# Performance work log

Measured on AMD Instinct MI355X. Metric: run time of the kernel, lower is better.

## Reference

```python
import jax, jax.numpy as jnp
import numpy as np

D, H, F, N, V, B, S, T = 512, 8, 2048, 2, 32000, 2, 1024, 1024


def _pe(seq_len, d):
    pos = np.arange(seq_len)[:, None].astype(np.float32)
    div = np.exp(np.arange(0, d, 2).astype(np.float32) * (-np.log(10000.0) / d))
    pe = np.zeros((seq_len, d), np.float32)
    pe[:, 0::2] = np.sin(pos * div)
    pe[:, 1::2] = np.cos(pos * div)
    return jnp.asarray(pe)


def _ln(x, g, b, eps=1e-6):
    # torch .var() default is unbiased (ddof=1)
    m = x.mean(-1, keepdims=True)
    v = jnp.sum((x - m) ** 2, -1, keepdims=True) / (x.shape[-1] - 1)
    return g * (x - m) / jnp.sqrt(v + eps) + b


def _mha(q, k, v, mask, w, b):
    # w: [4, D, D] (q,k,v,o); b: [4, D]
    Bq, Sq, Dm = q.shape
    Sk = k.shape[1]
    dk = Dm // H
    Q = (q @ w[0] + b[0]).reshape(Bq, Sq, H, dk).transpose(0, 2, 1, 3)
    K = (k @ w[1] + b[1]).reshape(Bq, Sk, H, dk).transpose(0, 2, 1, 3)
    Vv = (v @ w[2] + b[2]).reshape(Bq, Sk, H, dk).transpose(0, 2, 1, 3)
    s = jnp.einsum('bhqd,bhkd->bhqk', Q, K) / jnp.sqrt(jnp.float32(dk))
    s = jnp.where(mask == 0, jnp.float32(-1e9), s)
    a = jax.nn.softmax(s, axis=-1)
    o = jnp.einsum('bhqk,bhkd->bhqd', a, Vv).transpose(0, 2, 1, 3).reshape(Bq, Sq, Dm)
    return o @ w[3] + b[3]


def _ffn(x, w1, b1, w2, b2):
    return jax.nn.relu(x @ w1 + b1) @ w2 + b2


def _forward(src, tgt, src_mask, tgt_mask, p):
    (src_emb, tgt_emb, ea_w, ea_b, ef_w1, ef_b1, ef_w2, ef_b2, eln_g, eln_b, en_g, en_b,
     ds_w, ds_b, dc_w, dc_b, df_w1, df_b1, df_w2, df_b2, dln_g, dln_b, dn_g, dn_b, pw, pb) = p
    scale = jnp.sqrt(jnp.float32(D))
    # encoder
    x = src_emb[src] * scale + _pe(src.shape[1], D)
    for i in range(N):
        h = _ln(x, eln_g[i, 0], eln_b[i, 0])
        x = x + _mha(h, h, h, src_mask, ea_w[i], ea_b[i])
        h = _ln(x, eln_g[i, 1], eln_b[i, 1])
        x = x + _ffn(h, ef_w1[i], ef_b1[i], ef_w2[i], ef_b2[i])
    enc = _ln(x, en_g, en_b)
    # decoder
    y = tgt_emb[tgt] * scale + _pe(tgt.shape[1], D)
    for i in range(N):
        h = _ln(y, dln_g[i, 0], dln_b[i, 0])
        y = y + _mha(h, h, h, tgt_mask, ds_w[i], ds_b[i])
        h = _ln(y, dln_g[i, 1], dln_b[i, 1])
        y = y + _mha(h, enc, enc, src_mask, dc_w[i], dc_b[i])
        h = _ln(y, dln_g[i, 2], dln_b[i, 2])
        y = y + _ffn(h, df_w1[i], df_b1[i], df_w2[i], df_b2[i])
    y = _ln(y, dn_g, dn_b)
    return jax.nn.log_softmax(y @ pw + pb, axis=-1)


def setup_inputs() -> dict:
    key = jax.random.key(0)
    c = [0]
    def nk():
        c[0] += 1
        return jax.random.fold_in(key, c[0])
    def w(*s):
        return jax.random.normal(nk(), s, jnp.float32) * 0.02
    inp = {
        'src': jax.random.randint(nk(), (B, S), 0, V, jnp.int32),
        'tgt': jax.random.randint(nk(), (B, T), 0, V, jnp.int32),
        'src_mask': jnp.ones((B, 1, 1, S), jnp.int32),
        'tgt_mask': jnp.tril(jnp.ones((T, T), jnp.int32))[None, None],
        'src_emb': w(V, D), 'tgt_emb': w(V, D),
        'enc_attn_w': w(N, 4, D, D), 'enc_attn_b': jnp.zeros((N, 4, D), jnp.float32),
        'enc_ffn_w1': w(N, D, F), 'enc_ffn_b1': jnp.zeros((N, F), jnp.float32),
        'enc_ffn_w2': w(N, F, D), 'enc_ffn_b2': jnp.zeros((N, D), jnp.float32),
        'enc_ln_g': jnp.ones((N, 2, D), jnp.float32), 'enc_ln_b': jnp.zeros((N, 2, D), jnp.float32),
        'enc_norm_g': jnp.ones((D,), jnp.float32), 'enc_norm_b': jnp.zeros((D,), jnp.float32),
        'dec_self_w': w(N, 4, D, D), 'dec_self_b': jnp.zeros((N, 4, D), jnp.float32),
        'dec_cross_w': w(N, 4, D, D), 'dec_cross_b': jnp.zeros((N, 4, D), jnp.float32),
        'dec_ffn_w1': w(N, D, F), 'dec_ffn_b1': jnp.zeros((N, F), jnp.float32),
        'dec_ffn_w2': w(N, F, D), 'dec_ffn_b2': jnp.zeros((N, D), jnp.float32),
        'dec_ln_g': jnp.ones((N, 3, D), jnp.float32), 'dec_ln_b': jnp.zeros((N, 3, D), jnp.float32),
        'dec_norm_g': jnp.ones((D,), jnp.float32), 'dec_norm_b': jnp.zeros((D,), jnp.float32),
        'proj_w': w(D, V), 'proj_b': jnp.zeros((V,), jnp.float32),
    }
    return inp


def reference(src, tgt, src_mask, tgt_mask, src_emb, tgt_emb, enc_attn_w, enc_attn_b,
              enc_ffn_w1, enc_ffn_b1, enc_ffn_w2, enc_ffn_b2, enc_ln_g, enc_ln_b,
              enc_norm_g, enc_norm_b, dec_self_w, dec_self_b, dec_cross_w, dec_cross_b,
              dec_ffn_w1, dec_ffn_b1, dec_ffn_w2, dec_ffn_b2, dec_ln_g, dec_ln_b,
              dec_norm_g, dec_norm_b, proj_w, proj_b):
    p = (src_emb, tgt_emb, enc_attn_w, enc_attn_b, enc_ffn_w1, enc_ffn_b1, enc_ffn_w2,
         enc_ffn_b2, enc_ln_g, enc_ln_b, enc_norm_g, enc_norm_b, dec_self_w, dec_self_b,
         dec_cross_w, dec_cross_b, dec_ffn_w1, dec_ffn_b1, dec_ffn_w2, dec_ffn_b2,
         dec_ln_g, dec_ln_b, dec_norm_g, dec_norm_b, proj_w, proj_b)
    return _forward(src, tgt, src_mask, tgt_mask, p)
```

## Files before the change

### kernel.cpp

```cpp
#include <hip/hip_runtime.h>
#include <hip/hip_bf16.h>
#include <math.h>

using bf16 = __hip_bfloat16;
typedef float f32x4 __attribute__((ext_vector_type(4)));
typedef short short8 __attribute__((ext_vector_type(8)));

constexpr int kD = 512, kH = 8, kDk = 64, kF = 2048, kV = 32000;
constexpr int kB = 2, kS = 1024, kM = 2048, kBH = 16;

enum { ST_F32 = 0, ST_BF16, ST_QKV };

__device__ __forceinline__ void gload_lds16(const void* g, void* l) {
  __builtin_amdgcn_global_load_lds(
      (const __attribute__((address_space(1))) void*)g,
      (__attribute__((address_space(3))) void*)l, 16, 0, 0);
}

__device__ __forceinline__ float bfu2f(short u) {
  union { unsigned int i; float f; } c;
  c.i = ((unsigned int)(unsigned short)u) << 16;
  return c.f;
}

template <int BM, int BN, int STM, bool BIAS, bool RELU, bool RES, int NBUF, bool XSWZ, bool ASEL>
__launch_bounds__(256)
__global__ void k_gemm(const bf16* __restrict__ A, int lda, long long Az,
                       const bf16* __restrict__ Bt, int ldb, long long Bz,
                       void* __restrict__ Cv, int ldc, long long Cz,
                       int K, float alpha,
                       const float* __restrict__ bias,
                       const float* __restrict__ res,
                       const bf16* __restrict__ A2) {
  static_assert(NBUF == 1 || (BM == 64 && BN == 64), "pipeline path sized for 64x64");
  constexpr int FM = BM / 32, FN = BN / 32;
  __shared__ __attribute__((aligned(16))) bf16 As[NBUF][BM * 64];
  __shared__ __attribute__((aligned(16))) bf16 Bs[NBUF][BN * 64];
  const int tid = threadIdx.x;
  const int w = tid >> 6, lane = tid & 63;
  int bx = blockIdx.x, by = blockIdx.y;
  if constexpr (XSWZ) {
    const int nx = gridDim.x, ny = gridDim.y;
    const int lin = by * nx + bx;
    const int cpx = (nx * ny) >> 3;
    const int s = (lin & 7) * cpx + (lin >> 3);
    bx = s / ny;
    by = s - bx * ny;
  }
  const int bm = by * BM, bn = bx * BN;
  const int z = blockIdx.z;
  if constexpr (ASEL) { if (bn >= 512) A = A2; }
  A += (long long)z * Az;
  Bt += (long long)z * Bz;
  const int l15 = lane & 15, lhi = lane >> 4;
  const int wr = (w >> 1) * (BM / 2), wc = (w & 1) * (BN / 2);
  f32x4 acc[FM][FN] = {};
  const int nkt = K >> 6;

  auto stage = [&](int kt, int nb) {
#pragma unroll
    for (int it = 0; it < BM / 32; ++it) {
      int chunk = (it * 4 + w) * 64 + lane;
      int row = chunk >> 3, col = (chunk & 7) << 3;
      gload_lds16(A + (size_t)(bm + row) * lda + kt * 64 + col, As[nb] + (it * 4 + w) * 512);
    }
#pragma unroll
    for (int it = 0; it < BN / 32; ++it) {
      int chunk = (it * 4 + w) * 64 + lane;
      int row = chunk >> 3, col = (chunk & 7) << 3;
      gload_lds16(Bt + (size_t)(bn + row) * ldb + kt * 64 + col, Bs[nb] + (it * 4 + w) * 512);
    }
  };
  auto compute = [&](int cb) {
#pragma unroll
    for (int kk = 0; kk < 2; ++kk) {
      short8 af[FM], bf[FN];
#pragma unroll
      for (int i = 0; i < FM; ++i)
        af[i] = *(const short8*)(As[cb] + (wr + i * 16 + l15) * 64 + kk * 32 + lhi * 8);
#pragma unroll
      for (int j = 0; j < FN; ++j)
        bf[j] = *(const short8*)(Bs[cb] + (wc + j * 16 + l15) * 64 + kk * 32 + lhi * 8);
#pragma unroll
      for (int i = 0; i < FM; ++i)
#pragma unroll
        for (int j = 0; j < FN; ++j)
          acc[i][j] = __builtin_amdgcn_mfma_f32_16x16x32_bf16(af[i], bf[j], acc[i][j], 0, 0, 0);
    }
  };

  if constexpr (NBUF == 3) {
    stage(0, 0);
    stage(1, 1);
    stage(2, 2);
    asm volatile("s_waitcnt vmcnt(8)" ::: "memory");
    __builtin_amdgcn_s_barrier();
    __builtin_amdgcn_sched_barrier(0);
    int cur = 0;
    for (int kt = 0; kt < nkt; ++kt) {
      compute(cur);
      asm volatile("s_waitcnt lgkmcnt(0)" ::: "memory");
      __builtin_amdgcn_sched_barrier(0);
      if (kt + 1 < nkt) {
        __builtin_amdgcn_s_barrier();
        if (kt + 3 < nkt) {
          stage(kt + 3, cur);
          asm volatile("s_waitcnt vmcnt(8)" ::: "memory");
        } else {
          asm volatile("s_waitcnt vmcnt(0)" ::: "memory");
        }
        __builtin_amdgcn_s_barrier();
        __builtin_amdgcn_sched_barrier(0);
      }
      cur = (cur == 2) ? 0 : cur + 1;
    }
  } else {
    for (int kt = 0; kt < nkt; ++kt) {
      stage(kt, 0);
      __syncthreads();
      compute(0);
      __syncthreads();
    }
  }

#pragma unroll
  for (int i = 0; i < FM; ++i) {
#pragma unroll
    for (int j = 0; j < FN; ++j) {
#pragma unroll
      for (int r = 0; r < 4; ++r) {
        int m = bm + wr + i * 16 + lhi * 4 + r;
        int n = bn + wc + j * 16 + l15;
        float val = acc[i][j][r] * alpha;
        if constexpr (BIAS) val += bias[n];
        if constexpr (RELU) val = fmaxf(val, 0.f);
        if constexpr (RES) val += res[(size_t)m * ldc + n];
        if constexpr (STM == ST_F32) {
          ((float*)Cv)[(size_t)z * Cz + (size_t)m * ldc + n] = val;
        } else if constexpr (STM == ST_BF16) {
          ((bf16*)Cv)[(size_t)z * Cz + (size_t)m * ldc + n] = __float2bfloat16(val);
        } else if constexpr (STM == ST_QKV) {
          int seg = n >> 9, nn = n & 511;
          int b_ = m >> 10, s_ = m & 1023, h_ = nn >> 6, d_ = nn & 63;
          size_t idx = (seg < 2)
              ? (((size_t)(b_ * kH + h_) << 10) + s_) * kDk + d_
              : ((size_t)(b_ * kH + h_) * kDk + d_) * kS + s_;
          ((bf16*)Cv)[(size_t)seg * 1048576 + idx] = __float2bfloat16(val);
        }
      }
    }
  }
}

template <bool CAUSAL>
__launch_bounds__(256)
__global__ void k_fattn(const bf16* __restrict__ Q, const bf16* __restrict__ K,
                        const bf16* __restrict__ Vt, bf16* __restrict__ O) {
  __shared__ __attribute__((aligned(16))) bf16 Ks[3][4096];
  __shared__ __attribute__((aligned(16))) bf16 Vs[3][4096];
  __shared__ __attribute__((aligned(16))) bf16 Ps[4][1024];
  const int tid = threadIdx.x, w = tid >> 6, lane = tid & 63;
  const int l15 = lane & 15, lhi = lane >> 4;
  const int q0 = blockIdx.x * 64, bh = blockIdx.y;
  const int qw = q0 + w * 16;
  const bf16* Qp = Q + (((size_t)(bh << 10)) + qw + l15) * kDk;
  short8 aq[2];
  aq[0] = *(const short8*)(Qp + lhi * 8);
  aq[1] = *(const short8*)(Qp + 32 + lhi * 8);
  const int srow = w * 8 + (lane >> 3);
  const int sc = (lane & 7) ^ (srow & 7);
  const bf16* Ksrc = K + (((size_t)(bh << 10)) + srow) * kDk + sc * 8;
  const bf16* Vsrc = Vt + ((size_t)bh * kDk + srow) * kS + sc * 8;
  const int nt = CAUSAL ? (q0 >> 6) + 1 : (kS >> 6);

  auto stage = [&](int t, int nb) {
    int kv0 = t << 6;
    gload_lds16(Ksrc + (size_t)kv0 * kDk, Ks[nb] + w * 512);
    gload_lds16(Ksrc + (size_t)(kv0 + 32) * kDk, Ks[nb] + 2048 + w * 512);
    gload_lds16(Vsrc + kv0, Vs[nb] + w * 512);
    gload_lds16(Vsrc + kv0 + 32 * kS, Vs[nb] + 2048 + w * 512);
  };

  float m_[4], l_[4];
#pragma unroll
  for (int r = 0; r < 4; ++r) { m_[r] = -1e30f; l_[r] = 0.f; }
  f32x4 ao[4] = {};

  stage(0, 0);
  if (nt > 2) {
    stage(1, 1);
    stage(2, 2);
    asm volatile("s_waitcnt vmcnt(8)" ::: "memory");
  } else if (nt > 1) {
    stage(1, 1);
    asm volatile("s_waitcnt vmcnt(4)" ::: "memory");
  } else {
    asm volatile("s_waitcnt vmcnt(0)" ::: "memory");
  }
  __builtin_amdgcn_s_barrier();
  __builtin_amdgcn_sched_barrier(0);

  int cur = 0;
  for (int t = 0; t < nt; ++t) {
    f32x4 as[4] = {};
#pragma unroll
    for (int kk = 0; kk < 2; ++kk) {
      short8 bk[4];
#pragma unroll
      for (int nf = 0; nf < 4; ++nf) {
        int row = nf * 16 + l15;
        int c = (4 * kk + lhi) ^ (row & 7);
        bk[nf] = *(const short8*)(Ks[cur] + row * 64 + c * 8);
      }
#pragma unroll
      for (int nf = 0; nf < 4; ++nf)
        as[nf] = __builtin_amdgcn_mfma_f32_16x16x32_bf16(aq[kk], bk[nf], as[nf], 0, 0, 0);
    }
    float s[4][4];
#pragma unroll
    for (int nf = 0; nf < 4; ++nf)
#pragma unroll
      for (int r = 0; r < 4; ++r) {
        float v = as[nf][r] * 0.125f;
        if (CAUSAL && t == nt - 1) {
          int col = (t << 6) + nf * 16 + l15;
          int row = qw + lhi * 4 + r;
          if (col > row) v = -1e30f;
        }
        s[nf][r] = v;
      }
    float mn[4], scl[4], rsum[4];
#pragma unroll
    for (int r = 0; r < 4; ++r) {
      float mx = fmaxf(fmaxf(s[0][r], s[1][r]), fmaxf(s[2][r], s[3][r]));
      mx = fmaxf(mx, __shfl_xor(mx, 1));
      mx = fmaxf(mx, __shfl_xor(mx, 2));
      mx = fmaxf(mx, __shfl_xor(mx, 4));
      mx = fmaxf(mx, __shfl_xor(mx, 8));
      mn[r] = fmaxf(m_[r], mx);
      scl[r] = __expf(m_[r] - mn[r]);
      rsum[r] = 0.f;
    }
#pragma unroll
    for (int nf = 0; nf < 4; ++nf)
#pragma unroll
      for (int r = 0; r < 4; ++r) {
        float p = __expf(s[nf][r] - mn[r]);
        rsum[r] += p;
        int pr = lhi * 4 + r;
        int c = (2 * nf + (l15 >> 3)) ^ (pr & 7);
        Ps[w][pr * 64 + c * 8 + (l15 & 7)] = __float2bfloat16(p);
      }
#pragma unroll
    for (int r = 0; r < 4; ++r) {
      float su = rsum[r];
      su += __shfl_xor(su, 1);
      su += __shfl_xor(su, 2);
      su += __shfl_xor(su, 4);
      su += __shfl_xor(su, 8);
      l_[r] = l_[r] * scl[r] + su;
      m_[r] = mn[r];
    }
#pragma unroll
    for (int nf = 0; nf < 4; ++nf)
#pragma unroll
      for (int r = 0; r < 4; ++r) ao[nf][r] *= scl[r];
    asm volatile("s_waitcnt lgkmcnt(0)" ::: "memory");
    __builtin_amdgcn_sched_barrier(0);
#pragma unroll
    for (int kk = 0; kk < 2; ++kk) {
      short8 pa = *(const short8*)(Ps[w] + l15 * 64 + (((4 * kk + lhi) ^ (l15 & 7)) * 8));
      short8 bv[4];
#pragma unroll
      for (int nf = 0; nf < 4; ++nf) {
        int row = nf * 16 + l15;
        int c = (4 * kk + lhi) ^ (row & 7);
        bv[nf] = *(const short8*)(Vs[cur] + row * 64 + c * 8);
      }
#pragma unroll
      for (int nf = 0; nf < 4; ++nf)
        ao[nf] = __builtin_amdgcn_mfma_f32_16x16x32_bf16(pa, bv[nf], ao[nf], 0, 0, 0);
    }
    asm volatile("s_waitcnt lgkmcnt(0)" ::: "memory");
    __builtin_amdgcn_sched_barrier(0);
    if (t + 1 < nt) {
      __builtin_amdgcn_s_barrier();
      if (t + 3 < nt) {
        stage(t + 3, cur);
        asm volatile("s_waitcnt vmcnt(8)" ::: "memory");
      } else {
        asm volatile("s_waitcnt vmcnt(0)" ::: "memory");
      }
      __builtin_amdgcn_s_barrier();
      __builtin_amdgcn_sched_barrier(0);
    }
    cur = (cur == 2) ? 0 : cur + 1;
  }
  const int b_ = bh >> 3, h_ = bh & 7;
  float inv[4];
#pragma unroll
  for (int r = 0; r < 4; ++r) inv[r] = 1.f / l_[r];
#pragma unroll
  for (int nf = 0; nf < 4; ++nf)
#pragma unroll
    for (int r = 0; r < 4; ++r) {
      int q = qw + lhi * 4 + r;
      O[((size_t)(b_ * kS + q)) * kD + h_ * kDk + nf * 16 + l15] =
          __float2bfloat16(ao[nf][r] * inv[r]);
    }
}

struct TJobs {
  const float* src[8];
  bf16* dst[8];
  int K[8], N[8];
  int ofs[9];
};

__global__ void k_transpose_all(TJobs J) {
  __shared__ float t[32][33];
  const int tb = blockIdx.x;
  int j = 0;
#pragma unroll
  for (int i = 1; i < 8; ++i) j += (tb >= J.ofs[i]) ? 1 : 0;
  const int K = J.K[j], N = J.N[j];
  const int tn = N >> 5, tk = K >> 5;
  int r = tb - J.ofs[j];
  const int z = r / (tn * tk);
  r -= z * tn * tk;
  const int k0 = (r / tn) << 5, n0 = (r % tn) << 5;
  const float* Wp = J.src[j] + (size_t)z * K * N;
  bf16* WTp = J.dst[j] + (size_t)z * K * N;
  const int tx = threadIdx.x, ty = threadIdx.y;
#pragma unroll
  for (int rr = 0; rr < 32; rr += 8) t[ty + rr][tx] = Wp[(size_t)(k0 + ty + rr) * N + n0 + tx];
  __syncthreads();
#pragma unroll
  for (int rr = 0; rr < 32; rr += 8)
    WTp[(size_t)(n0 + ty + rr) * K + k0 + tx] = __float2bfloat16(t[tx][ty + rr]);
}

__global__ void k_embed2(const int* __restrict__ src, const int* __restrict__ tgt,
                         const float* __restrict__ se, const float* __restrict__ te,
                         float* __restrict__ xe, float* __restrict__ xd) {
  const int m = blockIdx.x, which = blockIdx.y;
  const int* tok = which ? tgt : src;
  const float* emb = which ? te : se;
  float* x = which ? xd : xe;
  int s = m & (kS - 1);
  const float* e = emb + (size_t)tok[m] * kD;
  float* xp = x + (size_t)m * kD;
  for (int d = threadIdx.x; d < kD; d += 256) {
    int i = d >> 1;
    float freq = __expf(-(float)(2 * i) * (9.210340371976184f / 512.0f));
    float ang = (float)s * freq;
    float pe = (d & 1) ? cosf(ang) : sinf(ang);
    xp[d] = e[d] * 22.62741699796952f + pe;
  }
}

__global__ void k_ln(const float* __restrict__ x, const float* __restrict__ g,
                     const float* __restrict__ b, bf16* __restrict__ out) {
  int w = threadIdx.x >> 6, lane = threadIdx.x & 63;
  int row = blockIdx.x * 4 + w;
  const float* xp = x + (size_t)row * kD;
  float v[8];
  float sum = 0.f;
#pragma unroll
  for (int i = 0; i < 8; ++i) { v[i] = xp[lane + i * 64]; sum += v[i]; }
#pragma unroll
  for (int o = 32; o; o >>= 1) sum += __shfl_xor(sum, o);
  float mean = sum * (1.f / 512.f);
  float sq = 0.f;
#pragma unroll
  for (int i = 0; i < 8; ++i) { float d = v[i] - mean; sq += d * d; }
#pragma unroll
  for (int o = 32; o; o >>= 1) sq += __shfl_xor(sq, o);
  float inv = rsqrtf(sq * (1.f / 511.f) + 1e-6f);
  bf16* op = out + (size_t)row * kD;
#pragma unroll
  for (int i = 0; i < 8; ++i) {
    int d = lane + i * 64;
    op[d] = __float2bfloat16(g[d] * (v[i] - mean) * inv + b[d]);
  }
}

__global__ __launch_bounds__(640, 2) void k_lsm_bf(const bf16* __restrict__ L,
                                                   float* __restrict__ y) {
  const bf16* row = L + (size_t)blockIdx.x * kV;
  float* orow = y + (size_t)blockIdx.x * kV;
  const int t = threadIdx.x;
  const bool extra = t < 160;
  float v[56];
  float sum = 0.f;
#pragma unroll
  for (int i = 0; i < 6; ++i) {
    short8 s = *(const short8*)(row + (t + i * 640) * 8);
#pragma unroll
    for (int e = 0; e < 8; ++e) {
      float f = bfu2f(s[e]);
      v[i * 8 + e] = f;
      sum += __expf(f);
    }
  }
  if (extra) {
    short8 s = *(const short8*)(row + (3840 + t) * 8);
#pragma unroll
    for (int e = 0; e < 8; ++e) {
      float f = bfu2f(s[e]);
      v[48 + e] = f;
      sum += __expf(f);
    }
  }
#pragma unroll
  for (int o = 32; o; o >>= 1) sum += __shfl_xor(sum, o);
  __shared__ float red2[10];
  const int w = t >> 6, lane = t & 63;
  if (lane == 0) red2[w] = sum;
  __syncthreads();
  sum = 0.f;
#pragma unroll
  for (int i = 0; i < 10; ++i) sum += red2[i];
  const float sh = logf(sum);
#pragma unroll
  for (int i = 0; i < 6; ++i)
#pragma unroll
    for (int e = 0; e < 8; ++e) orow[(t + i * 640) * 8 + e] = v[i * 8 + e] - sh;
  if (extra)
#pragma unroll
    for (int e = 0; e < 8; ++e) orow[(3840 + t) * 8 + e] = v[48 + e] - sh;
}

extern "C" void kernel_launch(void* const* d_in, const int* in_sizes, int n_in,
                              void* d_out, int out_size, void* d_ws, size_t ws_size,
                              hipStream_t stream) {
  (void)in_sizes; (void)n_in; (void)out_size;
  if (ws_size < (size_t)212 * 1024 * 1024) return;

  const int* src = (const int*)d_in[0];
  const int* tgt = (const int*)d_in[1];
  const float* src_emb   = (const float*)d_in[4];
  const float* tgt_emb   = (const float*)d_in[5];
  const float* enc_attn_w = (const float*)d_in[6];
  const float* enc_attn_b = (const float*)d_in[7];
  const float* enc_ffn_w1 = (const float*)d_in[8];
  const float* enc_ffn_b1 = (const float*)d_in[9];
  const float* enc_ffn_w2 = (const float*)d_in[10];
  const float* enc_ffn_b2 = (const float*)d_in[11];
  const float* enc_ln_g  = (const float*)d_in[12];
  const float* enc_ln_b  = (const float*)d_in[13];
  const float* enc_norm_g = (const float*)d_in[14];
  const float* enc_norm_b = (const float*)d_in[15];
  const float* dec_self_w = (const float*)d_in[16];
  const float* dec_self_b = (const float*)d_in[17];
  const float* dec_cross_w = (const float*)d_in[18];
  const float* dec_cross_b = (const float*)d_in[19];
  const float* dec_ffn_w1 = (const float*)d_in[20];
  const float* dec_ffn_b1 = (const float*)d_in[21];
  const float* dec_ffn_w2 = (const float*)d_in[22];
  const float* dec_ffn_b2 = (const float*)d_in[23];
  const float* dec_ln_g  = (const float*)d_in[24];
  const float* dec_ln_b  = (const float*)d_in[25];
  const float* dec_norm_g = (const float*)d_in[26];
  const float* dec_norm_b = (const float*)d_in[27];
  const float* proj_w    = (const float*)d_in[28];
  const float* proj_b    = (const float*)d_in[29];

  char* ws = (char*)d_ws;
  auto MB = [](size_t x) { return x << 20; };
  bf16* enc_attn_wt  = (bf16*)(ws + MB(0));
  bf16* dec_self_wt  = (bf16*)(ws + MB(4));
  bf16* dec_cross_wt = (bf16*)(ws + MB(8));
  bf16* enc_f1t = (bf16*)(ws + MB(12));
  bf16* enc_f2t = (bf16*)(ws + MB(16));
  bf16* dec_f1t = (bf16*)(ws + MB(20));
  bf16* dec_f2t = (bf16*)(ws + MB(24));
  bf16* proj_wt = (bf16*)(ws + MB(28));
  float* x_enc  = (float*)(ws + MB(60));
  float* x_dec  = (float*)(ws + MB(64));
  bf16* hbuf    = (bf16*)(ws + MB(68));
  bf16* enc_bf  = (bf16*)(ws + MB(70));
  bf16* Qb      = (bf16*)(ws + MB(72));
  bf16* attn_o  = (bf16*)(ws + MB(78));
  bf16* logits  = (bf16*)(ws + MB(80));
  bf16* ffn_mid = (bf16*)d_out;

  TJobs tj;
  int acc = 0;
  auto setj = [&](int j, const float* s, bf16* d, int K, int N, int z) {
    tj.src[j] = s; tj.dst[j] = d; tj.K[j] = K; tj.N[j] = N; tj.ofs[j] = acc;
    acc += (K >> 5) * (N >> 5) * z;
  };
  setj(0, enc_attn_w, enc_attn_wt, 512, 512, 8);
  setj(1, dec_self_w, dec_self_wt, 512, 512, 8);
  setj(2, dec_cross_w, dec_cross_wt, 512, 512, 8);
  setj(3, enc_ffn_w1, enc_f1t, 512, 2048, 2);
  setj(4, enc_ffn_w2, enc_f2t, 2048, 512, 2);
  setj(5, dec_ffn_w1, dec_f1t, 512, 2048, 2);
  setj(6, dec_ffn_w2, dec_f2t, 2048, 512, 2);
  setj(7, proj_w, proj_wt, 512, 32000, 1);
  tj.ofs[8] = acc;
  k_transpose_all<<<acc, dim3(32, 8), 0, stream>>>(tj);

  k_embed2<<<dim3(kM, 2), 256, 0, stream>>>(src, tgt, src_emb, tgt_emb, x_enc, x_dec);

  auto LN = [&](const float* x, const float* g, const float* b, bf16* out) {
    k_ln<<<kM / 4, 256, 0, stream>>>(x, g, b, out);
  };
  auto out_proj = [&](const bf16* wt, const float* bias, float* xio) {
    k_gemm<64, 64, ST_F32, true, false, true, 3, false, false><<<dim3(8, 32, 1), 256, 0, stream>>>(
        attn_o, 512, 0, wt + 3 * 262144, 512, 0, xio, 512, 0, 512, 1.f, bias + 3 * 512, xio, nullptr);
  };
  auto self_attn = [&](const bf16* wt, const float* bias, bool causal, float* xio) {
    k_gemm<64, 64, ST_QKV, true, false, false, 3, false, false><<<dim3(24, 32, 1), 256, 0, stream>>>(
        hbuf, 512, 0, wt, 512, 0, Qb, 0, 0, 512, 1.f, bias, nullptr, nullptr);
    if (causal) k_fattn<true><<<dim3(16, kBH), 256, 0, stream>>>(Qb, Qb + 1048576, Qb + 2097152, attn_o);
    else        k_fattn<false><<<dim3(16, kBH), 256, 0, stream>>>(Qb, Qb + 1048576, Qb + 2097152, attn_o);
    out_proj(wt, bias, xio);
  };
  auto cross_attn = [&](const bf16* wt, const float* bias, float* xio) {
    k_gemm<64, 64, ST_QKV, true, false, false, 3, false, true><<<dim3(24, 32, 1), 256, 0, stream>>>(
        hbuf, 512, 0, wt, 512, 0, Qb, 0, 0, 512, 1.f, bias, nullptr, enc_bf);
    k_fattn<false><<<dim3(16, kBH), 256, 0, stream>>>(Qb, Qb + 1048576, Qb + 2097152, attn_o);
    out_proj(wt, bias, xio);
  };
  auto ffn_block = [&](float* xio, const bf16* w1t, const float* b1, const bf16* w2t,
                       const float* b2, const float* g, const float* bl) {
    LN(xio, g, bl, hbuf);
    k_gemm<64, 64, ST_BF16, true, true, false, 3, false, false><<<dim3(32, 32, 1), 256, 0, stream>>>(
        hbuf, 512, 0, w1t, 512, 0, ffn_mid, kF, 0, 512, 1.f, b1, nullptr, nullptr);
    k_gemm<64, 64, ST_F32, true, false, true, 3, false, false><<<dim3(8, 32, 1), 256, 0, stream>>>(
        ffn_mid, 2048, 0, w2t, 2048, 0, xio, 512, 0, 2048, 1.f, b2, xio, nullptr);
  };

  for (int i = 0; i < 2; ++i) {
    LN(x_enc, enc_ln_g + i * 1024, enc_ln_b + i * 1024, hbuf);
    self_attn(enc_attn_wt + (size_t)i * 1048576, enc_attn_b + i * 2048, false, x_enc);
    ffn_block(x_enc, enc_f1t + (size_t)i * 1048576, enc_ffn_b1 + i * 2048,
              enc_f2t + (size_t)i * 1048576, enc_ffn_b2 + i * 512,
              enc_ln_g + i * 1024 + 512, enc_ln_b + i * 1024 + 512);
  }
  LN(x_enc, enc_norm_g, enc_norm_b, enc_bf);

  for (int i = 0; i < 2; ++i) {
    LN(x_dec, dec_ln_g + i * 1536, dec_ln_b + i * 1536, hbuf);
    self_attn(dec_self_wt + (size_t)i * 1048576, dec_self_b + i * 2048, true, x_dec);
    LN(x_dec, dec_ln_g + i * 1536 + 512, dec_ln_b + i * 1536 + 512, hbuf);
    cross_attn(dec_cross_wt + (size_t)i * 1048576, dec_cross_b + i * 2048, x_dec);
    ffn_block(x_dec, dec_f1t + (size_t)i * 1048576, dec_ffn_b1 + i * 2048,
              dec_f2t + (size_t)i * 1048576, dec_ffn_b2 + i * 512,
              dec_ln_g + i * 1536 + 1024, dec_ln_b + i * 1536 + 1024);
  }
  LN(x_dec, dec_norm_g, dec_norm_b, hbuf);

  k_gemm<128, 128, ST_BF16, true, false, false, 1, true, false><<<dim3(250, 16, 1), 256, 0, stream>>>(
      hbuf, 512, 0, proj_wt, 512, 0, logits, kV, 0, 512, 1.f, proj_b, nullptr, nullptr);
  k_lsm_bf<<<kM, 640, 0, stream>>>(logits, (float*)d_out);
}
```

Baseline: 734.5 us.

## Add dedicated 256x256-tile projection GEMM with 4-stage LDS pipeline

Replaces the generic 128x128 GEMM for the vocabulary projection with a specialized kernel that uses 256x256 tiles, 512 threads, and a 4-buffer global-to-LDS async pipeline with swizzled layout. Block indices are remapped so that blocks sharing rows or columns run close together. The larger tiles are meant to raise arithmetic intensity and operand reuse on the biggest GEMM (2048x32000x512). In exchange the kernel launches fewer blocks (1000), needs high register use at one block per CU, and relies on hardcoded shapes.

Result: no change. 726.8 us (-1.1%).

```diff
diff --git a/kernel.cpp b/kernel.cpp
--- a/kernel.cpp
+++ b/kernel.cpp
@@ -150,6 +150,77 @@
       }
     }
   }
+}
+
+__global__ __launch_bounds__(512, 1) void k_proj256(const bf16* __restrict__ A,
+                                                    const bf16* __restrict__ Bt,
+                                                    bf16* __restrict__ C,
+                                                    const float* __restrict__ bias) {
+  __shared__ __attribute__((aligned(16))) bf16 As[4][256 * 32];
+  __shared__ __attribute__((aligned(16))) bf16 Bs[4][256 * 32];
+  const int tid = threadIdx.x, w = tid >> 6, lane = tid & 63;
+  const int l15 = lane & 15, lhi = lane >> 4;
+  const int lin = blockIdx.y * 125 + blockIdx.x;
+  const int s = (lin & 7) * 125 + (lin >> 3);
+  const int bx = s >> 3, by = s & 7;
+  const int bm = by * 256, bn = bx * 256;
+  const int wr = (w >> 2) * 128, wc = (w & 3) * 64;
+  const int rowq = tid >> 2, chk = tid & 3;
+  const int swz = (chk ^ ((rowq >> 1) & 3)) << 3;
+  const bf16* Asrc0 = A + (size_t)(bm + rowq) * kD + swz;
+  const bf16* Asrc1 = A + (size_t)(bm + 128 + rowq) * kD + swz;
+  const bf16* Bsrc0 = Bt + (size_t)(bn + rowq) * kD + swz;
+  const bf16* Bsrc1 = Bt + (size_t)(bn + 128 + rowq) * kD + swz;
+  const int ldsoff = w * 1024;
+
+  auto stage = [&](int kt) {
+    const int b = kt & 3;
+    const int ko = kt * 32;
+    gload_lds16(Asrc0 + ko, (char*)As[b] + ldsoff);
+    gload_lds16(Asrc1 + ko, (char*)As[b] + 8192 + ldsoff);
+    gload_lds16(Bsrc0 + ko, (char*)Bs[b] + ldsoff);
+    gload_lds16(Bsrc1 + ko, (char*)Bs[b] + 8192 + ldsoff);
+  };
+
+  const int ra = wr + l15, rb = wc + l15;
+  const int abase = ra * 64 + ((lhi ^ ((ra >> 1) & 3)) << 4);
+  const int bbase = rb * 64 + ((lhi ^ ((rb >> 1) & 3)) << 4);
+
+  f32x4 acc[8][4] = {};
+  stage(0); stage(1); stage(2);
+  for (int kt = 0; kt < 16; ++kt) {
+    if (kt + 2 < 16)      asm volatile("s_waitcnt vmcnt(8)" ::: "memory");
+    else if (kt + 1 < 16) asm volatile("s_waitcnt vmcnt(4)" ::: "memory");
+    else                  asm volatile("s_waitcnt vmcnt(0)" ::: "memory");
+    __builtin_amdgcn_s_barrier();
+    __builtin_amdgcn_sched_barrier(0);
+    if (kt + 3 < 16) stage(kt + 3);
+    const int b = kt & 3;
+    short8 af[8], bf[4];
+#pragma unroll
+    for (int i = 0; i < 8; ++i)
+      af[i] = *(const short8*)((const char*)As[b] + abase + i * 1024);
+#pragma unroll
+    for (int j = 0; j < 4; ++j)
+      bf[j] = *(const short8*)((const char*)Bs[b] + bbase + j * 1024);
+#pragma unroll
+    for (int i = 0; i < 8; ++i)
+#pragma unroll
+      for (int j = 0; j < 4; ++j)
+        acc[i][j] = __builtin_amdgcn_mfma_f32_16x16x32_bf16(af[i], bf[j], acc[i][j], 0, 0, 0);
+    asm volatile("s_waitcnt lgkmcnt(0)" ::: "memory");
+    __builtin_amdgcn_sched_barrier(0);
+  }
+#pragma unroll
+  for (int i = 0; i < 8; ++i)
+#pragma unroll
+    for (int j = 0; j < 4; ++j)
+#pragma unroll
+      for (int r = 0; r < 4; ++r) {
+        int m = bm + wr + i * 16 + lhi * 4 + r;
+        int n = bn + wc + j * 16 + l15;
+        C[(size_t)m * kV + n] = __float2bfloat16(acc[i][j][r] + bias[n]);
+      }
 }
 
 template <bool CAUSAL>
@@ -553,7 +624,6 @@
   }
   LN(x_dec, dec_norm_g, dec_norm_b, hbuf);
 
-  k_gemm<128, 128, ST_BF16, true, false, false, 1, true, false><<<dim3(250, 16, 1), 256, 0, stream>>>(
-      hbuf, 512, 0, proj_wt, 512, 0, logits, kV, 0, 512, 1.f, proj_b, nullptr, nullptr);
+  k_proj256<<<dim3(125, 8), 512, 0, stream>>>(hbuf, proj_wt, logits, proj_b);
   k_lsm_bf<<<kM, 640, 0, stream>>>(logits, (float*)d_out);
 }
```
